# Optimization experiments

Hardware: AMD Instinct MI355X
Metric: run time of the kernel (lower is better)

## Reference

```python
import jax, jax.numpy as jnp
from jax import lax
import numpy as np

# GConv2d config (matches init_kwargs)
OUT_TRANSFORMS = 4  # rotations: 0, 90, 180, 270 degrees
STRIDE = 1
PADDING = 1


def setup_inputs() -> dict:
    key = jax.random.key(0)
    k1, k2, k3, k4 = jax.random.split(key, 4)
    B, IC_EFF, H, W = 16, 256, 64, 64   # IC_EFF = in_channels * in_transformations
    OC, K, F = 64, 4, 3                 # out_channels, num_dynamic_kernels, filter_size
    x = jax.random.normal(k1, (B, IC_EFF, H, W), dtype=jnp.float32)
    W_fc = jax.random.normal(k2, (K, IC_EFF), dtype=jnp.float32) * (1.0 / np.sqrt(IC_EFF))
    b_fc = jnp.zeros((K,), dtype=jnp.float32)
    kernel_bank = jax.random.normal(k3, (K, OC, IC_EFF, F, F), dtype=jnp.float32)
    return {"x": x, "W_fc": W_fc, "b_fc": b_fc, "kernel_bank": kernel_bank}


def reference(x, W_fc, b_fc, kernel_bank):
    B, C, H, W = x.shape
    # Dynamic routing: global average pool -> linear -> softmax over kernel bank
    pooled = x.mean(axis=(2, 3))                      # [B, C]
    coeffs = jax.nn.softmax(pooled @ W_fc.T + b_fc, axis=1)  # [B, K]
    # Sample-specific base kernels: mix of kernel bank
    base = jnp.einsum('bk,kocij->bocij', coeffs, kernel_bank)  # [B, oc, C, f, f]
    # P4 orientation expansion: rotate kernel spatially, stack along out-channels
    oriented = jnp.concatenate(
        [jnp.rot90(base, k, axes=(-2, -1)) for k in range(OUT_TRANSFORMS)], axis=1
    )  # [B, 4*oc, C, f, f]
    O, f = oriented.shape[1], oriented.shape[-1]
    # Batched per-sample conv via grouped convolution (one launch instead of B)
    xg = x.reshape(1, B * C, H, W)
    kg = oriented.reshape(B * O, C, f, f)
    out = lax.conv_general_dilated(
        xg, kg,
        window_strides=(STRIDE, STRIDE),
        padding=[(PADDING, PADDING), (PADDING, PADDING)],
        dimension_numbers=('NCHW', 'OIHW', 'NCHW'),
        feature_group_count=B,
    )  # [1, B*O, H', W']
    Ho, Wo = out.shape[-2], out.shape[-1]
    return out.reshape(B, O, Ho, Wo)
```

## Files before the change

kernel.cpp:

```cpp
#include <hip/hip_runtime.h>

#define B_  16
#define C_  256
#define O_  256

typedef short    bf16x8 __attribute__((ext_vector_type(8)));
typedef float    f32x16 __attribute__((ext_vector_type(16)));
typedef unsigned u32x4  __attribute__((ext_vector_type(4)));

#define XROW_SH  1056
#define XBC_SH   (66 * XROW_SH)
#define XT_BYTES ((size_t)B_ * 16 * XBC_SH * 2)

#define WTILE_SH 9216
#define WORP_BYTES ((size_t)B_ * 16 * 4 * WTILE_SH * 2)

#define XBUF_SH  10752

__device__ __forceinline__ unsigned cvtpk(float lo, float hi) {
    unsigned r;
    asm("v_cvt_pk_bf16_f32 %0, %1, %2" : "=v"(r) : "v"(lo), "v"(hi));
    return r;
}

__device__ __forceinline__ void gload16(const void* g, void* l) {
    __builtin_amdgcn_global_load_lds(
        (const __attribute__((address_space(1))) unsigned int*)g,
        (__attribute__((address_space(3))) unsigned int*)l, 16, 0, 0);
}

__global__ __launch_bounds__(256) void xprep_kernel(const float* __restrict__ x,
                                                    short* __restrict__ xT,
                                                    float* __restrict__ pooled4) {
    const int cg = blockIdx.x;
    const int b  = blockIdx.y;
    const int z  = blockIdx.z;
    const int t  = threadIdx.x;
    const int lane = t & 63, wv = t >> 6;
    const int cc = cg >> 1, lh = cg & 1;

    short* xTb = xT + (size_t)(b * 16 + cc) * XBC_SH;
    const float* xb = x + ((size_t)(b * C_ + cg * 8) << 12);

    {
        u32x4 zv = {0, 0, 0, 0};
        if (t < 32) {
            int r   = z * 16 + 1 + (t >> 1);
            int col = (t & 1) ? 65 : 0;
            *(u32x4*)&xTb[r * XROW_SH + lh * 528 + col * 8] = zv;
        }
        if (z == 0 || z == 3) {
            int row = (z == 0) ? 0 : 65;
            if (t < 66) *(u32x4*)&xTb[row * XROW_SH + lh * 528 + t * 8] = zv;
        }
    }

    float s[8] = {0.f, 0.f, 0.f, 0.f, 0.f, 0.f, 0.f, 0.f};
    const int px = lane;
#pragma unroll
    for (int r = 0; r < 4; ++r) {
        const int row = z * 16 + wv * 4 + r;
        const float* src = xb + row * 64 + px;
        float v[8];
#pragma unroll
        for (int i = 0; i < 8; ++i) { v[i] = src[(size_t)i << 12]; s[i] += v[i]; }
        u32x4 d = { cvtpk(v[0], v[1]), cvtpk(v[2], v[3]),
                    cvtpk(v[4], v[5]), cvtpk(v[6], v[7]) };
        *(u32x4*)&xTb[(row + 1) * XROW_SH + lh * 528 + (px + 1) * 8] = d;
    }

#pragma unroll
    for (int i = 0; i < 8; ++i)
#pragma unroll
        for (int off = 32; off; off >>= 1) s[i] += __shfl_xor(s[i], off, 64);

    __shared__ float pr[4][8];
    if (lane == 0) {
#pragma unroll
        for (int i = 0; i < 8; ++i) pr[wv][i] = s[i];
    }
    __syncthreads();
    if (t < 8) {
        float v = pr[0][t] + pr[1][t] + pr[2][t] + pr[3][t];
        pooled4[(z * B_ + b) * C_ + cg * 8 + t] = v * (1.0f / 4096.0f);
    }
}

__global__ __launch_bounds__(256) void mix_kernel(const float* __restrict__ bank,
                                                  const float* __restrict__ pooled4,
                                                  const float* __restrict__ W_fc,
                                                  const float* __restrict__ b_fc,
                                                  short* __restrict__ worp) {
    const int cc = blockIdx.x;
    const int og = blockIdx.y;
    const int t  = threadIdx.x;

    __shared__ float bankL[4 * 16 * 16 * 10];
    __shared__ float cfs[16][4];

    for (int i = t; i < 4 * 16 * 16 * 9; i += 256) {
        int k  = i / 2304, r = i % 2304;
        int oc = r / 144,  r2 = r % 144;
        int c  = r2 / 9,   tap = r2 % 9;
        bankL[((k * 16 + oc) * 16 + c) * 10 + tap] =
            bank[(((size_t)k * 64 + og * 16 + oc) * C_ + cc * 16 + c) * 9 + tap];
    }
    if (t < 64) {
        int b = t >> 2, k = t & 3;
        float s = b_fc[k];
        for (int c = 0; c < C_; ++c) {
            float pv = pooled4[b * C_ + c] + pooled4[(B_ + b) * C_ + c]
                     + pooled4[(2 * B_ + b) * C_ + c] + pooled4[(3 * B_ + b) * C_ + c];
            s += pv * W_fc[k * C_ + c];
        }
        cfs[b][k] = s;
    }
    __syncthreads();
    if (t < 16) {
        float l0 = cfs[t][0], l1 = cfs[t][1], l2 = cfs[t][2], l3 = cfs[t][3];
        float mx = fmaxf(fmaxf(l0, l1), fmaxf(l2, l3));
        float e0 = expf(l0 - mx), e1 = expf(l1 - mx);
        float e2 = expf(l2 - mx), e3 = expf(l3 - mx);
        float inv = 1.f / (e0 + e1 + e2 + e3);
        cfs[t][0] = e0 * inv; cfs[t][1] = e1 * inv;
        cfs[t][2] = e2 * inv; cfs[t][3] = e3 * inv;
    }
    __syncthreads();

    const int oc_l = t & 15;
    const int lhs  = (t >> 4) & 1;
    const int bg   = t >> 5;
    const int o64  = og * 16 + oc_l;

#pragma unroll
    for (int bb = 0; bb < 2; ++bb) {
        const int b = bg * 2 + bb;
        const float c0 = cfs[b][0], c1 = cfs[b][1], c2 = cfs[b][2], c3 = cfs[b][3];
        float mixed[8][9];
#pragma unroll
        for (int ci = 0; ci < 8; ++ci) {
            const float* p0 = &bankL[((0 * 16 + oc_l) * 16 + lhs * 8 + ci) * 10];
            const float* p1 = p0 + 16 * 16 * 10;
            const float* p2 = p0 + 2 * 16 * 16 * 10;
            const float* p3 = p0 + 3 * 16 * 16 * 10;
#pragma unroll
            for (int tp = 0; tp < 9; ++tp)
                mixed[ci][tp] = c0 * p0[tp] + c1 * p1[tp] + c2 * p2[tp] + c3 * p3[tp];
        }
#pragma unroll
        for (int oq = 0; oq < 4; ++oq) {
#pragma unroll
            for (int td = 0; td < 9; ++td) {
                const int ti = td / 3, tj = td % 3;
                int si, sj;
                if      (oq == 0) { si = ti;     sj = tj;     }
                else if (oq == 1) { si = tj;     sj = 2 - ti; }
                else if (oq == 2) { si = 2 - ti; sj = 2 - tj; }
                else              { si = 2 - tj; sj = ti;     }
                const int ts = si * 3 + sj;
                u32x4 d = { cvtpk(mixed[0][ts], mixed[1][ts]),
                            cvtpk(mixed[2][ts], mixed[3][ts]),
                            cvtpk(mixed[4][ts], mixed[5][ts]),
                            cvtpk(mixed[6][ts], mixed[7][ts]) };
                size_t base = ((((((size_t)b * 16 + cc) * 4 + oq) * 9 + td) * 2
                                + lhs) * 64 + o64) * 8;
                *(u32x4*)&worp[base] = d;
            }
        }
    }
}

__global__ __launch_bounds__(256, 2)
void conv_mfma(const short* __restrict__ xT, const short* __restrict__ worp,
               float* __restrict__ out) {
    __shared__ short lds[2 * XBUF_SH + 2 * WTILE_SH];

    const int g    = blockIdx.x;
    const int w    = (g & 7) * 64 + (g >> 3);
    const int oq   = w & 3;
    const int m    = w >> 2;
    const int rowt = m & 7;
    const int b    = m >> 3;
    const int y0   = rowt * 8;

    const int t    = threadIdx.x;
    const int lane = t & 63;
    const int wid  = t >> 6;
    const int l31  = lane & 31;
    const int lh   = lane >> 5;

    const char* xsrcB = (const char*)xT
        + ((size_t)(b * 16) * XBC_SH + (size_t)y0 * XROW_SH) * 2 + lane * 16;
    const char* wsrcB = (const char*)worp
        + (((size_t)(b * 16) * 4) + oq) * (WTILE_SH * 2) + lane * 16;

#define STAGE(ccc, p)                                                           \
    { const char* xs = xsrcB + (size_t)(ccc) * (XBC_SH * 2);                    \
      const char* ws = wsrcB + (size_t)(ccc) * (4 * WTILE_SH * 2);              \
      char* xd = (char*)lds + (p) * (XBUF_SH * 2);                              \
      char* wd = (char*)lds + 2 * (XBUF_SH * 2) + (p) * (WTILE_SH * 2);         \
      for (int u = wid; u < 21; u += 4) gload16(xs + u * 1024, xd + u * 1024);  \
      for (int u = wid; u < 18; u += 4) gload16(ws + u * 1024, wd + u * 1024); }

#define BRD(r, s) (*(const bf16x8*)&xcur[(((r) * 2 + lh) * 66 + (s) + l31) * 8])
#define LOADROW(R, r)                                                           \
    { R[0] = BRD(r, 0);  R[1] = BRD(r, 1);  R[2] = BRD(r, 2);                   \
      R[3] = BRD(r, 32); R[4] = BRD(r, 33); R[5] = BRD(r, 34); }

#define TAPROW(i, RA, RB)                                                       \
    _Pragma("unroll")                                                           \
    for (int j = 0; j < 3; ++j) {                                               \
        const int tap = (i) * 3 + j;                                            \
        const short* wp = wcur + ((tap * 2 + lh) * 64 + l31) * 8;               \
        bf16x8 A0 = *(const bf16x8*)wp;                                         \
        bf16x8 A1 = *(const bf16x8*)(wp + 256);                                 \
        acc0[0] = __builtin_amdgcn_mfma_f32_32x32x16_bf16(A0, RA[j],     acc0[0], 0, 0, 0); \
        acc1[0] = __builtin_amdgcn_mfma_f32_32x32x16_bf16(A1, RA[j],     acc1[0], 0, 0, 0); \
        acc0[1] = __builtin_amdgcn_mfma_f32_32x32x16_bf16(A0, RA[3 + j], acc0[1], 0, 0, 0); \
        acc1[1] = __builtin_amdgcn_mfma_f32_32x32x16_bf16(A1, RA[3 + j], acc1[1], 0, 0, 0); \
        acc0[2] = __builtin_amdgcn_mfma_f32_32x32x16_bf16(A0, RB[j],     acc0[2], 0, 0, 0); \
        acc1[2] = __builtin_amdgcn_mfma_f32_32x32x16_bf16(A1, RB[j],     acc1[2], 0, 0, 0); \
        acc0[3] = __builtin_amdgcn_mfma_f32_32x32x16_bf16(A0, RB[3 + j], acc0[3], 0, 0, 0); \
        acc1[3] = __builtin_amdgcn_mfma_f32_32x32x16_bf16(A1, RB[3 + j], acc1[3], 0, 0, 0); \
    }

    f32x16 acc0[4] = {}, acc1[4] = {};

    STAGE(0, 0);
    __syncthreads();

    for (int cc = 0; cc < 16; ++cc) {
        const int p = cc & 1;
        const short* xcur = lds + p * XBUF_SH;
        const short* wcur = lds + 2 * XBUF_SH + p * WTILE_SH;

        bf16x8 Ra[6], Rb[6], Rc[6];
        LOADROW(Ra, 2 * wid);
        LOADROW(Rb, 2 * wid + 1);
        LOADROW(Rc, 2 * wid + 2);
        if (cc < 15) STAGE(cc + 1, p ^ 1);
        __builtin_amdgcn_s_setprio(1);
        TAPROW(0, Ra, Rb)
        __builtin_amdgcn_s_setprio(0);
        LOADROW(Ra, 2 * wid + 3);
        __builtin_amdgcn_s_setprio(1);
        TAPROW(1, Rb, Rc)
        TAPROW(2, Rc, Ra)
        __builtin_amdgcn_s_setprio(0);
        __syncthreads();
    }
#undef STAGE
#undef BRD
#undef LOADROW
#undef TAPROW

#pragma unroll
    for (int pf = 0; pf < 4; ++pf) {
        const int yb  = y0 + 2 * wid + (pf >> 1);
        const int xcb = 32 * (pf & 1) + l31;
#pragma unroll
        for (int r = 0; r < 16; ++r) {
            const int orow = (r & 3) + 8 * (r >> 2) + 4 * lh;
            const int o0   = oq * 64 + orow;
            __builtin_nontemporal_store(acc0[pf][r],
                &out[((size_t)(b * O_ + o0)      << 12) + yb * 64 + xcb]);
            __builtin_nontemporal_store(acc1[pf][r],
                &out[((size_t)(b * O_ + o0 + 32) << 12) + yb * 64 + xcb]);
        }
    }
}

extern "C" void kernel_launch(void* const* d_in, const int* in_sizes, int n_in,
                              void* d_out, int out_size, void* d_ws, size_t ws_size,
                              hipStream_t stream) {
    const float* x    = (const float*)d_in[0];
    const float* W_fc = (const float*)d_in[1];
    const float* b_fc = (const float*)d_in[2];
    const float* bank = (const float*)d_in[3];
    float* out = (float*)d_out;

    short* xTb     = (short*)d_ws;
    short* worp    = (short*)((char*)d_ws + XT_BYTES);
    float* pooled4 = (float*)((char*)d_ws + XT_BYTES + WORP_BYTES);

    xprep_kernel<<<dim3(32, 16, 4), 256, 0, stream>>>(x, xTb, pooled4);
    mix_kernel<<<dim3(16, 4), 256, 0, stream>>>(bank, pooled4, W_fc, b_fc, worp);
    conv_mfma<<<512, 256, 0, stream>>>(xTb, worp, out);
}
```

Measured before the change: 123.3 us.

## Spread mix kernel over more blocks and trim conv register rows

The mix kernel now runs on 256 blocks instead of 64, each handling 4 output channels. The FC dot product is split across all 256 threads with a shared-memory reduction, and the rotated-tap stores are divided between two thread halves. This targets the serial 256-iteration loop and the low block count in that tiny kernel. In the conv kernel, the next tile's staging is issued before the LDS row loads, and the three-row register rotation is replaced by two alternating buffers, which reduces register pressure at the cost of a more serial load-then-MFMA order.

```diff
diff --git a/kernel.cpp b/kernel.cpp
--- a/kernel.cpp
+++ b/kernel.cpp
@@ -95,25 +95,33 @@
     const int og = blockIdx.y;
     const int t  = threadIdx.x;
 
-    __shared__ float bankL[4 * 16 * 16 * 10];
+    __shared__ float bankL[4][4][16][10];
+    __shared__ float pl[64][4];
     __shared__ float cfs[16][4];
 
-    for (int i = t; i < 4 * 16 * 16 * 9; i += 256) {
-        int k  = i / 2304, r = i % 2304;
-        int oc = r / 144,  r2 = r % 144;
-        int c  = r2 / 9,   tap = r2 % 9;
-        bankL[((k * 16 + oc) * 16 + c) * 10 + tap] =
-            bank[(((size_t)k * 64 + og * 16 + oc) * C_ + cc * 16 + c) * 9 + tap];
-    }
-    if (t < 64) {
-        int b = t >> 2, k = t & 3;
-        float s = b_fc[k];
-        for (int c = 0; c < C_; ++c) {
+    for (int i = t; i < 2304; i += 256) {
+        int k  = i / 576, r = i % 576;
+        int oc = r / 144, r2 = r % 144;
+        int c  = r2 / 9,  tap = r2 % 9;
+        bankL[k][oc][c][tap] =
+            bank[(((size_t)k * 64 + og * 4 + oc) * C_ + cc * 16 + c) * 9 + tap];
+    }
+    {
+        int pair = t >> 2, seg = t & 3;
+        int b = pair >> 2, k = pair & 3;
+        float s = 0.f;
+        for (int ci = 0; ci < 64; ++ci) {
+            int c = seg * 64 + ci;
             float pv = pooled4[b * C_ + c] + pooled4[(B_ + b) * C_ + c]
                      + pooled4[(2 * B_ + b) * C_ + c] + pooled4[(3 * B_ + b) * C_ + c];
             s += pv * W_fc[k * C_ + c];
         }
-        cfs[b][k] = s;
+        pl[pair][seg] = s;
+    }
+    __syncthreads();
+    if (t < 64) {
+        int b = t >> 2, k = t & 3;
+        cfs[b][k] = pl[t][0] + pl[t][1] + pl[t][2] + pl[t][3] + b_fc[k];
     }
     __syncthreads();
     if (t < 16) {
@@ -127,47 +135,45 @@
     }
     __syncthreads();
 
-    const int oc_l = t & 15;
-    const int lhs  = (t >> 4) & 1;
-    const int bg   = t >> 5;
-    const int o64  = og * 16 + oc_l;
-
-#pragma unroll
-    for (int bb = 0; bb < 2; ++bb) {
-        const int b = bg * 2 + bb;
-        const float c0 = cfs[b][0], c1 = cfs[b][1], c2 = cfs[b][2], c3 = cfs[b][3];
-        float mixed[8][9];
-#pragma unroll
-        for (int ci = 0; ci < 8; ++ci) {
-            const float* p0 = &bankL[((0 * 16 + oc_l) * 16 + lhs * 8 + ci) * 10];
-            const float* p1 = p0 + 16 * 16 * 10;
-            const float* p2 = p0 + 2 * 16 * 16 * 10;
-            const float* p3 = p0 + 3 * 16 * 16 * 10;
-#pragma unroll
-            for (int tp = 0; tp < 9; ++tp)
-                mixed[ci][tp] = c0 * p0[tp] + c1 * p1[tp] + c2 * p2[tp] + c3 * p3[tp];
-        }
-#pragma unroll
-        for (int oq = 0; oq < 4; ++oq) {
-#pragma unroll
-            for (int td = 0; td < 9; ++td) {
-                const int ti = td / 3, tj = td % 3;
-                int si, sj;
-                if      (oq == 0) { si = ti;     sj = tj;     }
-                else if (oq == 1) { si = tj;     sj = 2 - ti; }
-                else if (oq == 2) { si = 2 - ti; sj = 2 - tj; }
-                else              { si = 2 - tj; sj = ti;     }
-                const int ts = si * 3 + sj;
-                u32x4 d = { cvtpk(mixed[0][ts], mixed[1][ts]),
-                            cvtpk(mixed[2][ts], mixed[3][ts]),
-                            cvtpk(mixed[4][ts], mixed[5][ts]),
-                            cvtpk(mixed[6][ts], mixed[7][ts]) };
-                size_t base = ((((((size_t)b * 16 + cc) * 4 + oq) * 9 + td) * 2
-                                + lhs) * 64 + o64) * 8;
-                *(u32x4*)&worp[base] = d;
-            }
-        }
-    }
+    const int oc_l = t & 3;
+    const int lhs  = (t >> 2) & 1;
+    const int b    = (t >> 3) & 15;
+    const int rep  = t >> 7;
+    const int o64  = og * 4 + oc_l;
+
+    const float c0 = cfs[b][0], c1 = cfs[b][1], c2 = cfs[b][2], c3 = cfs[b][3];
+    float mixed[8][9];
+#pragma unroll
+    for (int ci = 0; ci < 8; ++ci)
+#pragma unroll
+        for (int tp = 0; tp < 9; ++tp)
+            mixed[ci][tp] = c0 * bankL[0][oc_l][lhs * 8 + ci][tp]
+                          + c1 * bankL[1][oc_l][lhs * 8 + ci][tp]
+                          + c2 * bankL[2][oc_l][lhs * 8 + ci][tp]
+                          + c3 * bankL[3][oc_l][lhs * 8 + ci][tp];
+
+#define STOREOQ(OQ)                                                             \
+    _Pragma("unroll")                                                           \
+    for (int td = 0; td < 9; ++td) {                                            \
+        const int ti = td / 3, tj = td % 3;                                     \
+        int si, sj;                                                             \
+        if      ((OQ) == 0) { si = ti;     sj = tj;     }                       \
+        else if ((OQ) == 1) { si = tj;     sj = 2 - ti; }                       \
+        else if ((OQ) == 2) { si = 2 - ti; sj = 2 - tj; }                       \
+        else                { si = 2 - tj; sj = ti;     }                       \
+        const int ts = si * 3 + sj;                                             \
+        u32x4 d = { cvtpk(mixed[0][ts], mixed[1][ts]),                          \
+                    cvtpk(mixed[2][ts], mixed[3][ts]),                          \
+                    cvtpk(mixed[4][ts], mixed[5][ts]),                          \
+                    cvtpk(mixed[6][ts], mixed[7][ts]) };                        \
+        size_t base = ((((((size_t)b * 16 + cc) * 4 + (OQ)) * 9 + td) * 2       \
+                        + lhs) * 64 + o64) * 8;                                 \
+        *(u32x4*)&worp[base] = d;                                               \
+    }
+
+    if (rep == 0) { STOREOQ(0) STOREOQ(1) }
+    else          { STOREOQ(2) STOREOQ(3) }
+#undef STOREOQ
 }
 
 __global__ __launch_bounds__(256, 2)
@@ -231,21 +237,19 @@
 
     for (int cc = 0; cc < 16; ++cc) {
         const int p = cc & 1;
+        if (cc < 15) STAGE(cc + 1, p ^ 1);
         const short* xcur = lds + p * XBUF_SH;
         const short* wcur = lds + 2 * XBUF_SH + p * WTILE_SH;
 
-        bf16x8 Ra[6], Rb[6], Rc[6];
-        LOADROW(Ra, 2 * wid);
-        LOADROW(Rb, 2 * wid + 1);
-        LOADROW(Rc, 2 * wid + 2);
-        if (cc < 15) STAGE(cc + 1, p ^ 1);
+        bf16x8 R0[6], R1[6];
         __builtin_amdgcn_s_setprio(1);
-        TAPROW(0, Ra, Rb)
-        __builtin_amdgcn_s_setprio(0);
-        LOADROW(Ra, 2 * wid + 3);
-        __builtin_amdgcn_s_setprio(1);
-        TAPROW(1, Rb, Rc)
-        TAPROW(2, Rc, Ra)
+        LOADROW(R0, 2 * wid);
+        LOADROW(R1, 2 * wid + 1);
+        TAPROW(0, R0, R1)
+        LOADROW(R0, 2 * wid + 2)
+        TAPROW(1, R1, R0)
+        LOADROW(R1, 2 * wid + 3)
+        TAPROW(2, R0, R1)
         __builtin_amdgcn_s_setprio(0);
         __syncthreads();
     }
@@ -284,6 +288,6 @@
     float* pooled4 = (float*)((char*)d_ws + XT_BYTES + WORP_BYTES);
 
     xprep_kernel<<<dim3(32, 16, 4), 256, 0, stream>>>(x, xTb, pooled4);
-    mix_kernel<<<dim3(16, 4), 256, 0, stream>>>(bank, pooled4, W_fc, b_fc, worp);
+    mix_kernel<<<dim3(16, 16), 256, 0, stream>>>(bank, pooled4, W_fc, b_fc, worp);
     conv_mfma<<<512, 256, 0, stream>>>(xTb, worp, out);
 }
```

Result: faster. 105.9 us (-14.1%).
